# Performance work log

Measured on AMD Instinct MI355X. Metric: run time of the kernel, lower is better.

The kernel has to match this reference:

```python
import jax, jax.numpy as jnp
import numpy as np

B, L, D = 8, 512, 32      # batch, seq_len, hidden_size (input dim)
N = 64                     # features_nodes (attention neurons)
H = 64                     # interm_layer_size (LSTM hidden)


def setup_inputs() -> dict:
    key = jax.random.key(0)
    ks = jax.random.split(key, 12)
    s = lambda k, shape, fan: jax.random.normal(k, shape, jnp.float32) * (1.0 / np.sqrt(fan))
    return {
        "text": jax.random.normal(ks[0], (B, L, D), jnp.float32),
        # AttentionLSTM params
        "Wx_w": s(ks[1], (N, D), D),
        "Wx_b": jnp.zeros((N,), jnp.float32),
        "Wxhat_w": s(ks[2], (N, D), D),
        "Wxhat_b": jnp.zeros((N,), jnp.float32),
        "att_w": s(ks[3], (1, N), N),
        "att_b": jnp.zeros((1,), jnp.float32),
        # unidirectional LSTM params (PyTorch layout: gates i,f,g,o)
        "W_ih": s(ks[4], (4 * H, D), D),
        "W_hh": s(ks[5], (4 * H, H), H),
        "b_ih": jnp.zeros((4 * H,), jnp.float32),
        "b_hh": jnp.zeros((4 * H,), jnp.float32),
        # dense head
        "dense_w": s(ks[6], (2, H), H),
        "dense_b": jnp.zeros((2,), jnp.float32),
    }


def _forward(text, Wx_w, Wx_b, Wxhat_w, Wxhat_b, att_w, att_b,
             W_ih, W_hh, b_ih, b_hh, dense_w, dense_b):
    # --- AttentionLSTM ---
    Wx = text @ Wx_w.T + Wx_b          # [B,L,N]
    # Wthat[b,i,j,:] = text[b,j,:], so Linear(Wthat) == Wxhat broadcast over i
    Wxhat = text @ Wxhat_w.T + Wxhat_b  # [B,L,N]
    # tanh(Wxhat[b,j] + Wx[b,i]) -> [B,L,L,N]
    t = jnp.tanh(Wxhat[:, None, :, :] + Wx[:, :, None, :])
    A = jax.nn.sigmoid(jnp.einsum('bijn,n->bij', t, att_w[0]) + att_b[0])  # [B,L,L]
    Xatt = jnp.einsum('bij,bjd->bid', A, text)  # sum_j Wthat*A -> [B,L,D]

    # --- unidirectional LSTM (last hidden state only) ---
    h0 = jnp.zeros((text.shape[0], H), text.dtype)
    c0 = jnp.zeros((text.shape[0], H), text.dtype)

    def step(carry, x_t):
        h, c = carry
        gates = x_t @ W_ih.T + b_ih + h @ W_hh.T + b_hh  # [B,4H]
        i, f, g, o = jnp.split(gates, 4, axis=-1)
        c = jax.nn.sigmoid(f) * c + jax.nn.sigmoid(i) * jnp.tanh(g)
        h = jax.nn.sigmoid(o) * jnp.tanh(c)
        return (h, c), None

    (h_last, _), _ = jax.lax.scan(step, (h0, c0), jnp.swapaxes(Xatt, 0, 1))
    return h_last @ dense_w.T + dense_b  # [B,2]


def reference(text, Wx_w, Wx_b, Wxhat_w, Wxhat_b, att_w, att_b,
              W_ih, W_hh, b_ih, b_hh, dense_w, dense_b):
    return _forward(text, Wx_w, Wx_b, Wxhat_w, Wxhat_b, att_w, att_b,
                    W_ih, W_hh, b_ih, b_hh, dense_w, dense_b)
```

## Files before the change

### kernel.cpp

```cpp
#include <hip/hip_runtime.h>
#include <hip/hip_bf16.h>

#define Bb 8
#define Ll 512
#define Dd 32
#define Nn 64
#define Hh 64
#define G4 256

#define L2E  1.4426950408889634f
#define L2E2 2.8853900817779268f

typedef _Float16 h2_t __attribute__((ext_vector_type(2)));

__device__ __forceinline__ float fast_rcp(float x) { return __builtin_amdgcn_rcpf(x); }
__device__ __forceinline__ float fast_exp2(float x) { return __builtin_amdgcn_exp2f(x); }

__device__ __forceinline__ float sig2(float x) {
    return fast_rcp(1.f + fast_exp2(-L2E * x));
}
__device__ __forceinline__ float tanh2(float x) {
    return fmaf(2.f, fast_rcp(1.f + fast_exp2(-L2E2 * x)), -1.f);
}

__device__ __forceinline__ float fdot2(h2_t a, h2_t b, float c) {
#if __has_builtin(__builtin_amdgcn_fdot2)
    return __builtin_amdgcn_fdot2(a, b, c, false);
#else
    return c + (float)a[0] * (float)b[0] + (float)a[1] * (float)b[1];
#endif
}

template<int CTRL>
__device__ __forceinline__ float quad_dpp(float v) {
    return __int_as_float(__builtin_amdgcn_mov_dpp(__float_as_int(v), CTRL, 0xf, 0xf, true));
}
__device__ __forceinline__ float quad_sum(float v) {
    v += quad_dpp<0xB1>(v);
    v += quad_dpp<0x4E>(v);
    return v;
}

__global__ __launch_bounds__(256) void k_proj(
    const float* __restrict__ text,
    const float* __restrict__ Wx_w, const float* __restrict__ Wx_b,
    const float* __restrict__ Wxh_w, const float* __restrict__ Wxh_b,
    float* __restrict__ Ex, float* __restrict__ Eh) {
    int idx = blockIdx.x * 256 + threadIdx.x;
    int n = idx & 63;
    int bl = idx >> 6;
    const float4* tr = (const float4*)(text + bl * Dd);
    const float4* w1 = (const float4*)(Wx_w + n * Dd);
    const float4* w2 = (const float4*)(Wxh_w + n * Dd);
    float a0 = 0.f, a1 = 0.f;
#pragma unroll
    for (int q = 0; q < 8; ++q) {
        float4 t4 = tr[q]; float4 x4 = w1[q]; float4 y4 = w2[q];
        a0 += t4.x * x4.x + t4.y * x4.y + t4.z * x4.z + t4.w * x4.w;
        a1 += t4.x * y4.x + t4.y * y4.y + t4.z * y4.z + t4.w * y4.w;
    }
    Ex[idx] = fast_exp2(L2E2 * (a0 + Wx_b[n]));
    Eh[idx] = fast_exp2(L2E2 * (a1 + Wxh_b[n]));
}

__global__ __launch_bounds__(256) void k_attn(
    const float* __restrict__ text,
    const float* __restrict__ Ex, const float* __restrict__ Eh,
    const float* __restrict__ att_w, const float* __restrict__ att_b,
    float* __restrict__ Xatt) {
    __shared__ float s_eh[64 * 65];
    __shared__ float s_text[32 * 65];
    __shared__ float2 s_fa[4 * 64];
    __shared__ float s_A[4 * 64];

    int tid = threadIdx.x;
    int bx = blockIdx.x;
    int b = bx >> 7;
    int i0 = (bx & 127) << 2;
    int w = tid >> 6, l = tid & 63;
    int i = i0 + w;

    s_fa[w * 64 + l] = make_float2(Ex[((b * Ll) + i) * Nn + l], att_w[l]);
    float ab = att_b[0];
    __syncthreads();

    float awsum = 0.f;
#pragma unroll
    for (int n = 0; n < 64; ++n) awsum += s_fa[w * 64 + n].y;
    float zc = awsum + ab;

    float xacc = 0.f;
    int d = l & 31, hf = l >> 5;

    for (int jt = 0; jt < 8; ++jt) {
        __syncthreads();
        {
            int n = tid & 63; int j4 = tid >> 6;
#pragma unroll
            for (int r = 0; r < 16; ++r) {
                int jl = j4 + r * 4;
                s_eh[n * 65 + jl] = Eh[((b * Ll) + jt * 64 + jl) * Nn + n];
            }
            int dd = tid & 31; int j8 = tid >> 5;
#pragma unroll
            for (int r = 0; r < 8; ++r) {
                int jl = j8 + r * 8;
                s_text[dd * 65 + jl] = text[((b * Ll) + jt * 64 + jl) * Dd + dd];
            }
        }
        __syncthreads();
        float S = 0.f;
#pragma unroll
        for (int n = 0; n < 64; ++n) {
            float E = s_eh[n * 65 + l];
            float2 fa = s_fa[w * 64 + n];
            float r = fast_rcp(fmaf(E, fa.x, 1.f));
            S = fmaf(fa.y, r, S);
        }
        float A = fast_rcp(1.f + fast_exp2(-L2E * (zc - 2.f * S)));
        s_A[w * 64 + l] = A;
#pragma unroll
        for (int jj = 0; jj < 32; ++jj) {
            int j = hf * 32 + jj;
            xacc += s_A[w * 64 + j] * s_text[d * 65 + j];
        }
    }
    xacc += __shfl_xor(xacc, 32);
    if (l < 32) Xatt[((b * Ll) + i) * Dd + l] = xacc;
}

__global__ __launch_bounds__(256) void k_gx(
    const float* __restrict__ Xatt,
    const float* __restrict__ W_ih, const float* __restrict__ b_ih,
    const float* __restrict__ b_hh, float* __restrict__ Gx) {
    int idx = blockIdx.x * 256 + threadIdx.x;
    int g = idx & 255, bt = idx >> 8;
    const float4* xr = (const float4*)(Xatt + bt * Dd);
    const float4* wr = (const float4*)(W_ih + g * Dd);
    float a = b_ih[g] + b_hh[g];
#pragma unroll
    for (int q = 0; q < 8; ++q) {
        float4 x4 = xr[q], w4 = wr[q];
        a += x4.x * w4.x + x4.y * w4.y + x4.z * w4.z + x4.w * w4.w;
    }
    Gx[idx] = a;
}

__global__ __launch_bounds__(256) void k_lstm(
    const float* __restrict__ Gx, const float* __restrict__ W_hh,
    const float* __restrict__ dense_w, const float* __restrict__ dense_b,
    float* __restrict__ out) {
    __shared__ __align__(16) _Float16 s_h[2][64];
    int b = blockIdx.x;
    int tid = threadIdx.x;
    int w = tid >> 6, l = tid & 63;
    int p = l & 3;
    int u = w * 16 + (l >> 2);

    h2_t wreg[4][8];
#pragma unroll
    for (int g = 0; g < 4; ++g) {
        const float4* wp = (const float4*)(W_hh + (g * 64 + u) * 64 + p * 16);
#pragma unroll
        for (int q = 0; q < 4; ++q) {
            float4 v = wp[q];
            wreg[g][2 * q]     = h2_t{(_Float16)v.x, (_Float16)v.y};
            wreg[g][2 * q + 1] = h2_t{(_Float16)v.z, (_Float16)v.w};
        }
    }

    if (tid < 64) s_h[0][tid] = (_Float16)0.f;
    float c = 0.f;
    const float* gxb = Gx + b * Ll * G4;
    int gidx = p * 64 + u;
    float gx_cur = gxb[gidx];
    float gx_n1  = gxb[G4 + gidx];
    __syncthreads();

    int buf = 0;
    for (int t = 0; t < Ll; ++t) {
        int t2 = (t + 2 < Ll) ? (t + 2) : (Ll - 1);
        float gx_n2 = gxb[t2 * G4 + gidx];

        union { float4 f; h2_t h[4]; } u0, u1;
        u0.f = *(const float4*)(&s_h[buf][p * 16]);
        u1.f = *(const float4*)(&s_h[buf][p * 16 + 8]);

        float a0 = (p == 0) ? gx_cur : 0.f;
        float a1 = (p == 1) ? gx_cur : 0.f;
        float a2 = (p == 2) ? gx_cur : 0.f;
        float a3 = (p == 3) ? gx_cur : 0.f;
#pragma unroll
        for (int q = 0; q < 4; ++q) {
            a0 = fdot2(u0.h[q], wreg[0][q], a0);
            a1 = fdot2(u0.h[q], wreg[1][q], a1);
            a2 = fdot2(u0.h[q], wreg[2][q], a2);
            a3 = fdot2(u0.h[q], wreg[3][q], a3);
        }
#pragma unroll
        for (int q = 0; q < 4; ++q) {
            a0 = fdot2(u1.h[q], wreg[0][q + 4], a0);
            a1 = fdot2(u1.h[q], wreg[1][q + 4], a1);
            a2 = fdot2(u1.h[q], wreg[2][q + 4], a2);
            a3 = fdot2(u1.h[q], wreg[3][q + 4], a3);
        }
        float ti = quad_sum(a0);
        float tf = quad_sum(a1);
        float tg = quad_sum(a2);
        float to = quad_sum(a3);

        float gi = sig2(ti);
        float gf = sig2(tf);
        float gg = tanh2(tg);
        float go = sig2(to);
        c = fmaf(gf, c, gi * gg);
        float hh = go * tanh2(c);
        if (p == 0) s_h[buf ^ 1][u] = (_Float16)hh;
        __syncthreads();
        buf ^= 1;
        gx_cur = gx_n1;
        gx_n1 = gx_n2;
    }
    if (tid == 0) {
        float a0 = dense_b[0], a1 = dense_b[1];
        for (int uu = 0; uu < 64; ++uu) {
            float hv = (float)s_h[buf][uu];
            a0 += hv * dense_w[uu];
            a1 += hv * dense_w[64 + uu];
        }
        out[b * 2 + 0] = a0;
        out[b * 2 + 1] = a1;
    }
}

extern "C" void kernel_launch(void* const* d_in, const int* in_sizes, int n_in,
                              void* d_out, int out_size, void* d_ws, size_t ws_size,
                              hipStream_t stream) {
    const float* text    = (const float*)d_in[0];
    const float* Wx_w    = (const float*)d_in[1];
    const float* Wx_b    = (const float*)d_in[2];
    const float* Wxh_w   = (const float*)d_in[3];
    const float* Wxh_b   = (const float*)d_in[4];
    const float* att_w   = (const float*)d_in[5];
    const float* att_b   = (const float*)d_in[6];
    const float* W_ih    = (const float*)d_in[7];
    const float* W_hh    = (const float*)d_in[8];
    const float* b_ih    = (const float*)d_in[9];
    const float* b_hh    = (const float*)d_in[10];
    const float* dense_w = (const float*)d_in[11];
    const float* dense_b = (const float*)d_in[12];

    float* ws   = (float*)d_ws;
    float* Ex   = ws;
    float* Eh   = ws + 262144;
    float* Xatt = ws + 524288;
    float* Gx   = ws + 655360;
    float* out  = (float*)d_out;

    hipLaunchKernelGGL(k_proj, dim3((Bb * Ll * Nn) / 256), dim3(256), 0, stream,
                       text, Wx_w, Wx_b, Wxh_w, Wxh_b, Ex, Eh);
    hipLaunchKernelGGL(k_attn, dim3(Bb * (Ll / 4)), dim3(256), 0, stream,
                       text, Ex, Eh, att_w, att_b, Xatt);
    hipLaunchKernelGGL(k_gx, dim3((Bb * Ll * G4) / 256), dim3(256), 0, stream,
                       Xatt, W_ih, b_ih, b_hh, Gx);
    hipLaunchKernelGGL(k_lstm, dim3(Bb), dim3(256), 0, stream,
                       Gx, W_hh, dense_w, dense_b, out);
}
```

Before: 219.0 us.

## Fuse input-gate projection into attention kernel and split LSTM gate activations across lanes

The separate W_ih projection kernel is folded into the end of the attention kernel. Each block writes its four Xatt rows to shared memory and computes their 256 gate pre-activations with register-held W_ih rows, which removes one launch and the Xatt global round trip. In the LSTM step, each lane of a quad now evaluates only one gate nonlinearity (sigmoid or tanh, chosen by per-lane constants) and the four values are broadcast with DPP quad permutes, instead of every lane computing all four. This shortens the serial per-step critical path but adds cross-lane permutes and depends on the existing quad_dpp helper.

New measurement: 203.2 us. -7.2%, faster.

```diff
diff --git a/kernel.cpp b/kernel.cpp
--- a/kernel.cpp
+++ b/kernel.cpp
@@ -67,11 +67,13 @@
     const float* __restrict__ text,
     const float* __restrict__ Ex, const float* __restrict__ Eh,
     const float* __restrict__ att_w, const float* __restrict__ att_b,
-    float* __restrict__ Xatt) {
+    const float* __restrict__ W_ih, const float* __restrict__ b_ih,
+    const float* __restrict__ b_hh, float* __restrict__ Gx) {
     __shared__ float s_eh[64 * 65];
     __shared__ float s_text[32 * 65];
     __shared__ float2 s_fa[4 * 64];
     __shared__ float s_A[4 * 64];
+    __shared__ __align__(16) float s_xatt[4][32];
 
     int tid = threadIdx.x;
     int bx = blockIdx.x;
@@ -126,24 +128,28 @@
         }
     }
     xacc += __shfl_xor(xacc, 32);
-    if (l < 32) Xatt[((b * Ll) + i) * Dd + l] = xacc;
-}
-
-__global__ __launch_bounds__(256) void k_gx(
-    const float* __restrict__ Xatt,
-    const float* __restrict__ W_ih, const float* __restrict__ b_ih,
-    const float* __restrict__ b_hh, float* __restrict__ Gx) {
-    int idx = blockIdx.x * 256 + threadIdx.x;
-    int g = idx & 255, bt = idx >> 8;
-    const float4* xr = (const float4*)(Xatt + bt * Dd);
-    const float4* wr = (const float4*)(W_ih + g * Dd);
-    float a = b_ih[g] + b_hh[g];
-#pragma unroll
-    for (int q = 0; q < 8; ++q) {
-        float4 x4 = xr[q], w4 = wr[q];
-        a += x4.x * w4.x + x4.y * w4.y + x4.z * w4.z + x4.w * w4.w;
-    }
-    Gx[idx] = a;
+    if (l < 32) s_xatt[w][l] = xacc;
+    __syncthreads();
+
+    {
+        int g = tid;
+        const float4* wr = (const float4*)(W_ih + g * Dd);
+        float4 wv[8];
+#pragma unroll
+        for (int q = 0; q < 8; ++q) wv[q] = wr[q];
+        float bias = b_ih[g] + b_hh[g];
+#pragma unroll
+        for (int r = 0; r < 4; ++r) {
+            const float4* xr = (const float4*)s_xatt[r];
+            float acc = bias;
+#pragma unroll
+            for (int q = 0; q < 8; ++q) {
+                float4 x4 = xr[q]; float4 w4 = wv[q];
+                acc += x4.x * w4.x + x4.y * w4.y + x4.z * w4.z + x4.w * w4.w;
+            }
+            Gx[((b * Ll) + i0 + r) * G4 + g] = acc;
+        }
+    }
 }
 
 __global__ __launch_bounds__(256) void k_lstm(
@@ -157,6 +163,10 @@
     int p = l & 3;
     int u = w * 16 + (l >> 2);
 
+    float pm = (p == 2) ? -L2E2 : -L2E;
+    float mo = (p == 2) ? 2.f : 1.f;
+    float ao = (p == 2) ? -1.f : 0.f;
+
     h2_t wreg[4][8];
 #pragma unroll
     for (int g = 0; g < 4; ++g) {
@@ -208,13 +218,15 @@
         float tf = quad_sum(a1);
         float tg = quad_sum(a2);
         float to = quad_sum(a3);
-
-        float gi = sig2(ti);
-        float gf = sig2(tf);
-        float gg = tanh2(tg);
-        float go = sig2(to);
-        c = fmaf(gf, c, gi * gg);
-        float hh = go * tanh2(c);
+        float tot = (p & 2) ? ((p & 1) ? to : tg) : ((p & 1) ? tf : ti);
+        float val = fmaf(mo, fast_rcp(1.f + fast_exp2(pm * tot)), ao);
+        float vi = quad_dpp<0x00>(val);
+        float vf = quad_dpp<0x55>(val);
+        float vg = quad_dpp<0xAA>(val);
+        float vo = quad_dpp<0xFF>(val);
+
+        c = fmaf(vf, c, vi * vg);
+        float hh = vo * tanh2(c);
         if (p == 0) s_h[buf ^ 1][u] = (_Float16)hh;
         __syncthreads();
         buf ^= 1;
@@ -253,16 +265,13 @@
     float* ws   = (float*)d_ws;
     float* Ex   = ws;
     float* Eh   = ws + 262144;
-    float* Xatt = ws + 524288;
     float* Gx   = ws + 655360;
     float* out  = (float*)d_out;
 
     hipLaunchKernelGGL(k_proj, dim3((Bb * Ll * Nn) / 256), dim3(256), 0, stream,
                        text, Wx_w, Wx_b, Wxh_w, Wxh_b, Ex, Eh);
     hipLaunchKernelGGL(k_attn, dim3(Bb * (Ll / 4)), dim3(256), 0, stream,
-                       text, Ex, Eh, att_w, att_b, Xatt);
-    hipLaunchKernelGGL(k_gx, dim3((Bb * Ll * G4) / 256), dim3(256), 0, stream,
-                       Xatt, W_ih, b_ih, b_hh, Gx);
+                       text, Ex, Eh, att_w, att_b, W_ih, b_ih, b_hh, Gx);
     hipLaunchKernelGGL(k_lstm, dim3(Bb), dim3(256), 0, stream,
                        Gx, W_hh, dense_w, dense_b, out);
 }
```
